# Performance work log

Measured on AMD Instinct MI355X. Metric: run time of the kernel, lower is better.

## Reference

```python
import jax, jax.numpy as jnp
import numpy as np

EPS = 1e-8  # matches torch F.cosine_similarity eps


def setup_inputs() -> dict:
    key = jax.random.key(0)
    S, U, D = 2048, 10, 256  # speakers, utterances/speaker, embedding dim
    embeddings = jax.random.normal(key, (S * U, D), dtype=jnp.float32)
    labels = jnp.repeat(jnp.arange(S, dtype=jnp.int64), U)  # speaker-blocked, as the view() assumes
    return {"embeddings": embeddings, "labels": labels}


def reference(embeddings, labels):
    labels_np = np.asarray(labels)
    S = int(np.unique(labels_np).size)          # num_speakers (static)
    B, D = embeddings.shape
    U = B // S                                   # num_utterances
    E = embeddings.reshape(S, U, D)
    C = E.mean(axis=1)                           # (S, D) centroids
    En = E / jnp.maximum(jnp.linalg.norm(E, axis=-1, keepdims=True), EPS)
    Cn = C / jnp.maximum(jnp.linalg.norm(C, axis=-1, keepdims=True), EPS)
    sim = jnp.einsum('sud,kd->suk', En, Cn)      # (S, U, S) cosine similarities
    idx = jnp.arange(S)
    pos = sim[idx, :, idx]                       # (S, U) similarity to own centroid
    neg_mask = jnp.eye(S, dtype=bool)[:, None, :]  # mask out k == i
    neg = jnp.where(neg_mask, -jnp.inf, sim)
    lse = jax.nn.logsumexp(neg, axis=-1)         # (S, U)
    loss = jnp.mean(-pos + lse)
    return loss
```

## Files before the change

### kernel.cpp

```cpp
#include <hip/hip_runtime.h>
#include <math.h>

#define SS   2048
#define UU   10
#define DD   256
#define BB   (SS * UU)
#define EPSF 1e-8f

typedef __attribute__((ext_vector_type(8))) short   bf16x8;
typedef __attribute__((ext_vector_type(4))) float   floatx4;

__device__ static inline unsigned short f2bf(float f) {
    union { float f; unsigned u; } v; v.f = f;
    unsigned r = (v.u + 0x7FFFu + ((v.u >> 16) & 1u)) >> 16;
    return (unsigned short)r;
}

__device__ static inline void gl_lds16(const unsigned short* g, unsigned short* l) {
    __builtin_amdgcn_global_load_lds((const __attribute__((address_space(1))) void*)g,
                                     (__attribute__((address_space(3))) void*)l, 16, 0, 0);
}

__global__ __launch_bounds__(256) void prep_kernel(const float* __restrict__ E,
                                                   unsigned short* __restrict__ Enb,
                                                   unsigned short* __restrict__ Cnb) {
    const int s   = blockIdx.x;
    const int wid = threadIdx.x >> 6, lane = threadIdx.x & 63;
    __shared__ float cent[4][256];
    __shared__ float sred[256];

    float cp0 = 0.f, cp1 = 0.f, cp2 = 0.f, cp3 = 0.f;
    for (int u = wid; u < UU; u += 4) {
        const size_t roff = (size_t)(s * UU + u) * DD;
        float4 v = ((const float4*)(E + roff))[lane];
        float ssq = v.x * v.x + v.y * v.y + v.z * v.z + v.w * v.w;
#pragma unroll
        for (int off = 32; off; off >>= 1) ssq += __shfl_xor(ssq, off, 64);
        const float rinv = 1.0f / fmaxf(sqrtf(ssq), EPSF);
        ushort4 o;
        o.x = f2bf(v.x * rinv); o.y = f2bf(v.y * rinv);
        o.z = f2bf(v.z * rinv); o.w = f2bf(v.w * rinv);
        ((ushort4*)(Enb + roff))[lane] = o;
        cp0 += v.x; cp1 += v.y; cp2 += v.z; cp3 += v.w;
    }
    cent[wid][lane * 4 + 0] = cp0;
    cent[wid][lane * 4 + 1] = cp1;
    cent[wid][lane * 4 + 2] = cp2;
    cent[wid][lane * 4 + 3] = cp3;
    __syncthreads();

    const int d = threadIdx.x;
    const float c = (cent[0][d] + cent[1][d] + cent[2][d] + cent[3][d]) * 0.1f;
    sred[d] = c * c;
    __syncthreads();
#pragma unroll
    for (int off = 128; off; off >>= 1) {
        if (d < off) sred[d] += sred[d + off];
        __syncthreads();
    }
    const float rinv = 1.0f / fmaxf(sqrtf(sred[0]), EPSF);
    Cnb[(size_t)s * DD + d] = f2bf(c * rinv);
}

#define BM 256
#define BN 128
#define BK 64

__global__ __launch_bounds__(256, 2) void gemm_lse_kernel(const unsigned short* __restrict__ Enb,
                                                          const unsigned short* __restrict__ Cnb,
                                                          float* __restrict__ posArr,
                                                          float* __restrict__ sumexp) {
    __shared__ unsigned short As[BM * BK];
    __shared__ unsigned short Bs[BN * BK];

    const int tid  = threadIdx.x;
    const int wid  = tid >> 6, lane = tid & 63;
    const int l15  = lane & 15, quad = lane >> 4;
    const int wave_m = wid >> 1, wave_n = wid & 1;

    const int bn = blockIdx.x & 15;
    const int bm = blockIdx.x >> 4;
    const int row0 = bm * BM, n0 = bn * BN;

    const int rl  = lane >> 3;
    const int gl8 = ((lane & 7) ^ rl) * 8;
    const unsigned short* gp[12];
    unsigned short* lp[12];
#pragma unroll
    for (int i = 0; i < 12; ++i) {
        const int c = wid * 12 + i;
        if (c < 32) {
            gp[i] = Enb + (size_t)(row0 + c * 8 + rl) * DD + gl8;
            lp[i] = As + c * 512;
        } else {
            gp[i] = Cnb + (size_t)(n0 + (c - 32) * 8 + rl) * DD + gl8;
            lp[i] = Bs + (c - 32) * 512;
        }
    }

    const int swz8 = ((quad ^ (l15 & 7))) * 8;
    int aoff[8], boff[4];
#pragma unroll
    for (int mt = 0; mt < 8; ++mt) aoff[mt] = (wave_m * 128 + mt * 16 + l15) * BK + swz8;
#pragma unroll
    for (int nt = 0; nt < 4; ++nt) boff[nt] = (wave_n * 64 + nt * 16 + l15) * BK + swz8;

    floatx4 acc[8][4];
#pragma unroll
    for (int i = 0; i < 8; ++i)
#pragma unroll
        for (int j = 0; j < 4; ++j) acc[i][j] = (floatx4){0.f, 0.f, 0.f, 0.f};

    for (int k0 = 0; k0 < DD; k0 += BK) {
        __syncthreads();
#pragma unroll
        for (int i = 0; i < 12; ++i) gl_lds16(gp[i] + k0, lp[i]);
        __syncthreads();
#pragma unroll
        for (int ks = 0; ks < 2; ++ks) {
            const int kx = ks * 32;
            bf16x8 af[8], bfr[4];
#pragma unroll
            for (int mt = 0; mt < 8; ++mt) af[mt]  = *(const bf16x8*)(As + (aoff[mt] ^ kx));
#pragma unroll
            for (int nt = 0; nt < 4; ++nt) bfr[nt] = *(const bf16x8*)(Bs + (boff[nt] ^ kx));
#pragma unroll
            for (int mt = 0; mt < 8; ++mt)
#pragma unroll
                for (int nt = 0; nt < 4; ++nt)
                    acc[mt][nt] = __builtin_amdgcn_mfma_f32_16x16x32_bf16(af[mt], bfr[nt], acc[mt][nt], 0, 0, 0);
        }
    }

#pragma unroll
    for (int mt = 0; mt < 8; ++mt) {
        float rs[4] = {0.f, 0.f, 0.f, 0.f};
        const int growb = row0 + wave_m * 128 + mt * 16 + quad * 4;
#pragma unroll
        for (int nt = 0; nt < 4; ++nt) {
            const int col = n0 + wave_n * 64 + nt * 16 + l15;
#pragma unroll
            for (int r = 0; r < 4; ++r) {
                const int grow = growb + r;
                const float sim = acc[mt][nt][r];
                if (col == grow / UU) {
                    posArr[grow] = sim;
                } else {
                    rs[r] += __expf(sim);
                }
            }
        }
#pragma unroll
        for (int m = 1; m < 16; m <<= 1) {
#pragma unroll
            for (int r = 0; r < 4; ++r) rs[r] += __shfl_xor(rs[r], m, 64);
        }
        if (l15 == 0) {
#pragma unroll
            for (int r = 0; r < 4; ++r) atomicAdd(&sumexp[growb + r], rs[r]);
        }
    }
}

__global__ __launch_bounds__(1024) void finalize_kernel(const float* __restrict__ posArr,
                                                        const float* __restrict__ sumexp,
                                                        float* __restrict__ out) {
    __shared__ float sred[1024];
    const int tid = threadIdx.x;
    float t = 0.f;
    for (int r = tid; r < BB; r += 1024) t += logf(sumexp[r]) - posArr[r];
    sred[tid] = t;
    __syncthreads();
#pragma unroll
    for (int off = 512; off; off >>= 1) {
        if (tid < off) sred[tid] += sred[tid + off];
        __syncthreads();
    }
    if (tid == 0) out[0] = sred[0] / (float)BB;
}

extern "C" void kernel_launch(void* const* d_in, const int* in_sizes, int n_in,
                              void* d_out, int out_size, void* d_ws, size_t ws_size,
                              hipStream_t stream) {
    const float* E = (const float*)d_in[0];
    float* out = (float*)d_out;

    unsigned short* Enb = (unsigned short*)d_ws;
    unsigned short* Cnb = Enb + (size_t)BB * DD;
    float* posArr = (float*)(Cnb + (size_t)SS * DD);
    float* sumexp = posArr + BB;

    hipMemsetAsync(sumexp, 0, BB * sizeof(float), stream);

    prep_kernel<<<SS, 256, 0, stream>>>(E, Enb, Cnb);
    gemm_lse_kernel<<<(BB / BM) * (SS / BN), 256, 0, stream>>>(Enb, Cnb, posArr, sumexp);
    finalize_kernel<<<1, 1024, 0, stream>>>(posArr, sumexp, out);
}
```

Baseline: 122.2 us.

## Shrink GEMM tiles, fold memset into prep, parallelize finalize with atomics

```diff
diff --git a/kernel.cpp b/kernel.cpp
--- a/kernel.cpp
+++ b/kernel.cpp
@@ -23,11 +23,16 @@
 
 __global__ __launch_bounds__(256) void prep_kernel(const float* __restrict__ E,
                                                    unsigned short* __restrict__ Enb,
-                                                   unsigned short* __restrict__ Cnb) {
+                                                   unsigned short* __restrict__ Cnb,
+                                                   float* __restrict__ sumexp,
+                                                   float* __restrict__ out) {
     const int s   = blockIdx.x;
     const int wid = threadIdx.x >> 6, lane = threadIdx.x & 63;
     __shared__ float cent[4][256];
     __shared__ float sred[256];
+
+    if (threadIdx.x < UU) sumexp[s * UU + threadIdx.x] = 0.f;
+    if (s == 0 && threadIdx.x == 0) out[0] = 0.f;
 
     float cp0 = 0.f, cp1 = 0.f, cp2 = 0.f, cp3 = 0.f;
     for (int u = wid; u < UU; u += 4) {
@@ -62,14 +67,14 @@
     Cnb[(size_t)s * DD + d] = f2bf(c * rinv);
 }
 
-#define BM 256
+#define BM 128
 #define BN 128
-#define BK 64
+#define BK 32
 
-__global__ __launch_bounds__(256, 2) void gemm_lse_kernel(const unsigned short* __restrict__ Enb,
-                                                          const unsigned short* __restrict__ Cnb,
-                                                          float* __restrict__ posArr,
-                                                          float* __restrict__ sumexp) {
+__global__ __launch_bounds__(256) void gemm_lse_kernel(const unsigned short* __restrict__ Enb,
+                                                       const unsigned short* __restrict__ Cnb,
+                                                       float* __restrict__ posArr,
+                                                       float* __restrict__ sumexp) {
     __shared__ unsigned short As[BM * BK];
     __shared__ unsigned short Bs[BN * BK];
 
@@ -82,60 +87,58 @@
     const int bm = blockIdx.x >> 4;
     const int row0 = bm * BM, n0 = bn * BN;
 
-    const int rl  = lane >> 3;
-    const int gl8 = ((lane & 7) ^ rl) * 8;
-    const unsigned short* gp[12];
-    unsigned short* lp[12];
+    const int rl = lane >> 2;
+    const int gf = ((lane & 3) ^ ((rl >> 1) & 3)) * 8;
+    const unsigned short* gp[4];
+    unsigned short* lp[4];
 #pragma unroll
-    for (int i = 0; i < 12; ++i) {
-        const int c = wid * 12 + i;
-        if (c < 32) {
-            gp[i] = Enb + (size_t)(row0 + c * 8 + rl) * DD + gl8;
+    for (int i = 0; i < 4; ++i) {
+        const int c = wid * 4 + i;
+        if (c < 8) {
+            gp[i] = Enb + (size_t)(row0 + c * 16 + rl) * DD + gf;
             lp[i] = As + c * 512;
         } else {
-            gp[i] = Cnb + (size_t)(n0 + (c - 32) * 8 + rl) * DD + gl8;
-            lp[i] = Bs + (c - 32) * 512;
+            gp[i] = Cnb + (size_t)(n0 + (c - 8) * 16 + rl) * DD + gf;
+            lp[i] = Bs + (c - 8) * 512;
         }
     }
 
-    const int swz8 = ((quad ^ (l15 & 7))) * 8;
-    int aoff[8], boff[4];
+    const int fswz = (quad ^ ((l15 >> 1) & 3)) * 8;
+    int aoff[4], boff[4];
 #pragma unroll
-    for (int mt = 0; mt < 8; ++mt) aoff[mt] = (wave_m * 128 + mt * 16 + l15) * BK + swz8;
+    for (int t = 0; t < 4; ++t) {
+        aoff[t] = (wave_m * 64 + t * 16 + l15) * BK + fswz;
+        boff[t] = (wave_n * 64 + t * 16 + l15) * BK + fswz;
+    }
+
+    floatx4 acc[4][4];
 #pragma unroll
-    for (int nt = 0; nt < 4; ++nt) boff[nt] = (wave_n * 64 + nt * 16 + l15) * BK + swz8;
-
-    floatx4 acc[8][4];
-#pragma unroll
-    for (int i = 0; i < 8; ++i)
+    for (int i = 0; i < 4; ++i)
 #pragma unroll
         for (int j = 0; j < 4; ++j) acc[i][j] = (floatx4){0.f, 0.f, 0.f, 0.f};
 
     for (int k0 = 0; k0 < DD; k0 += BK) {
         __syncthreads();
 #pragma unroll
-        for (int i = 0; i < 12; ++i) gl_lds16(gp[i] + k0, lp[i]);
+        for (int i = 0; i < 4; ++i) gl_lds16(gp[i] + k0, lp[i]);
         __syncthreads();
+
+        bf16x8 af[4], bfr[4];
 #pragma unroll
-        for (int ks = 0; ks < 2; ++ks) {
-            const int kx = ks * 32;
-            bf16x8 af[8], bfr[4];
+        for (int t = 0; t < 4; ++t) af[t]  = *(const bf16x8*)(As + aoff[t]);
 #pragma unroll
-            for (int mt = 0; mt < 8; ++mt) af[mt]  = *(const bf16x8*)(As + (aoff[mt] ^ kx));
+        for (int t = 0; t < 4; ++t) bfr[t] = *(const bf16x8*)(Bs + boff[t]);
 #pragma unroll
-            for (int nt = 0; nt < 4; ++nt) bfr[nt] = *(const bf16x8*)(Bs + (boff[nt] ^ kx));
+        for (int mt = 0; mt < 4; ++mt)
 #pragma unroll
-            for (int mt = 0; mt < 8; ++mt)
-#pragma unroll
-                for (int nt = 0; nt < 4; ++nt)
-                    acc[mt][nt] = __builtin_amdgcn_mfma_f32_16x16x32_bf16(af[mt], bfr[nt], acc[mt][nt], 0, 0, 0);
-        }
+            for (int nt = 0; nt < 4; ++nt)
+                acc[mt][nt] = __builtin_amdgcn_mfma_f32_16x16x32_bf16(af[mt], bfr[nt], acc[mt][nt], 0, 0, 0);
     }
 
 #pragma unroll
-    for (int mt = 0; mt < 8; ++mt) {
+    for (int mt = 0; mt < 4; ++mt) {
         float rs[4] = {0.f, 0.f, 0.f, 0.f};
-        const int growb = row0 + wave_m * 128 + mt * 16 + quad * 4;
+        const int growb = row0 + wave_m * 64 + mt * 16 + quad * 4;
 #pragma unroll
         for (int nt = 0; nt < 4; ++nt) {
             const int col = n0 + wave_n * 64 + nt * 16 + l15;
@@ -162,21 +165,20 @@
     }
 }
 
-__global__ __launch_bounds__(1024) void finalize_kernel(const float* __restrict__ posArr,
-                                                        const float* __restrict__ sumexp,
-                                                        float* __restrict__ out) {
-    __shared__ float sred[1024];
+__global__ __launch_bounds__(256) void finalize_kernel(const float* __restrict__ posArr,
+                                                       const float* __restrict__ sumexp,
+                                                       float* __restrict__ out) {
+    __shared__ float sred[256];
     const int tid = threadIdx.x;
-    float t = 0.f;
-    for (int r = tid; r < BB; r += 1024) t += logf(sumexp[r]) - posArr[r];
-    sred[tid] = t;
+    const int r = blockIdx.x * 256 + tid;
+    sred[tid] = logf(sumexp[r]) - posArr[r];
     __syncthreads();
 #pragma unroll
-    for (int off = 512; off; off >>= 1) {
+    for (int off = 128; off; off >>= 1) {
         if (tid < off) sred[tid] += sred[tid + off];
         __syncthreads();
     }
-    if (tid == 0) out[0] = sred[0] / (float)BB;
+    if (tid == 0) atomicAdd(out, sred[0] * (1.0f / (float)BB));
 }
 
 extern "C" void kernel_launch(void* const* d_in, const int* in_sizes, int n_in,
@@ -190,9 +192,7 @@
     float* posArr = (float*)(Cnb + (size_t)SS * DD);
     float* sumexp = posArr + BB;
 
-    hipMemsetAsync(sumexp, 0, BB * sizeof(float), stream);
-
-    prep_kernel<<<SS, 256, 0, stream>>>(E, Enb, Cnb);
+    prep_kernel<<<SS, 256, 0, stream>>>(E, Enb, Cnb, sumexp, out);
     gemm_lse_kernel<<<(BB / BM) * (SS / BN), 256, 0, stream>>>(Enb, Cnb, posArr, sumexp);
-    finalize_kernel<<<1, 1024, 0, stream>>>(posArr, sumexp, out);
+    finalize_kernel<<<BB / 256, 256, 0, stream>>>(posArr, sumexp, out);
 }
```

New measurement: 115.5 us. -5.5%, faster.
